# Kernel optimization log

Measured on AMD Instinct MI355X. Metric: run time of the kernel, lower is better.

The kernel has to match this reference:

```python
import jax, jax.numpy as jnp
import numpy as np

INPUT_DIM, LATENT_DIM, HIDDEN_DIM, BATCH = 1024, 128, 1024, 32768


def setup_inputs() -> dict:
    key = jax.random.key(0)
    ks = jax.random.split(key, 12)
    s = 0.02
    x = (jax.random.uniform(ks[0], (BATCH, INPUT_DIM)) < 0.5).astype(jnp.float32)  # binary data
    eps = jax.random.normal(ks[1], (BATCH, LATENT_DIM), dtype=jnp.float32)
    return {
        "x": x,
        "eps": eps,
        "We1": jax.random.normal(ks[2], (INPUT_DIM, HIDDEN_DIM)) * s,
        "be1": jnp.zeros((HIDDEN_DIM,), jnp.float32),
        "Wmu": jax.random.normal(ks[3], (HIDDEN_DIM, LATENT_DIM)) * s,
        "bmu": jnp.zeros((LATENT_DIM,), jnp.float32),
        "Wls": jax.random.normal(ks[4], (HIDDEN_DIM, LATENT_DIM)) * s,
        "bls": jnp.zeros((LATENT_DIM,), jnp.float32),
        "Wd1": jax.random.normal(ks[5], (LATENT_DIM, HIDDEN_DIM)) * s,
        "bd1": jnp.zeros((HIDDEN_DIM,), jnp.float32),
        "Wd2": jax.random.normal(ks[6], (HIDDEN_DIM, INPUT_DIM)) * s,
        "bd2": jnp.zeros((INPUT_DIM,), jnp.float32),
    }


def reference(x, eps, We1, be1, Wmu, bmu, Wls, bls, Wd1, bd1, Wd2, bd2):
    # Encoder: one hidden ReLU layer, mu / logsigma heads
    h = jax.nn.relu(x @ We1 + be1)                      # [B, H]
    mu = h @ Wmu + bmu                                  # [B, L]
    logsigma = h @ Wls + bls                            # [B, L]
    # Reparameterization: z = sigma * eps + mu (vectorized diag(exp(logsigma)) @ eps)
    z = mu + jnp.exp(logsigma) * eps                    # [B, L]
    # Decoder: one hidden ReLU layer, sigmoid Bernoulli params
    hd = jax.nn.relu(z @ Wd1 + bd1)                     # [B, H]
    theta = jax.nn.sigmoid(hd @ Wd2 + bd2)              # [B, D]
    # Bernoulli log-likelihood: sum_j log(theta^x * (1-theta)^(1-x))
    log_px = jnp.sum(x * jnp.log(theta) + (1.0 - x) * jnp.log1p(-theta), axis=-1)  # [B]
    # KL(q||N(0,I)) = 0.5 * sum(sigma^2 + mu^2 - log(sigma^2) - 1)
    kl = 0.5 * jnp.sum(jnp.exp(2.0 * logsigma) + mu * mu - 2.0 * logsigma - 1.0, axis=-1)  # [B]
    return log_px - kl                                  # elbo_mc [B]
```

## Files before the change

kernel.cpp:

```cpp
#include <hip/hip_runtime.h>
#include <cstdint>
#include <cstddef>


typedef __bf16 bf16x8 __attribute__((ext_vector_type(8)));
typedef float f32x4 __attribute__((ext_vector_type(4)));

__device__ __forceinline__ unsigned short f32_to_bf16(float f) {
  unsigned int u = __float_as_uint(f);
  u += 0x7fffu + ((u >> 16) & 1u);
  return (unsigned short)(u >> 16);
}

__global__ void cast_bf16_k(const float* __restrict__ in,
                            unsigned short* __restrict__ out,
                            unsigned short* __restrict__ xbit, int n4) {
  int stride = gridDim.x * blockDim.x;
  for (int i = blockIdx.x * blockDim.x + threadIdx.x; i < n4; i += stride) {
    float4 v = reinterpret_cast<const float4*>(in)[i];
    ushort4 o = make_ushort4(f32_to_bf16(v.x), f32_to_bf16(v.y),
                             f32_to_bf16(v.z), f32_to_bf16(v.w));
    reinterpret_cast<ushort4*>(out)[i] = o;
    unsigned int nib = (v.x != 0.f ? 1u : 0u) | (v.y != 0.f ? 2u : 0u) |
                       (v.z != 0.f ? 4u : 0u) | (v.w != 0.f ? 8u : 0u);
    unsigned int n1 = __shfl_down(nib, 1, 64);
    unsigned int n2 = __shfl_down(nib, 2, 64);
    unsigned int n3 = __shfl_down(nib, 3, 64);
    if ((threadIdx.x & 3) == 0)
      xbit[i >> 2] = (unsigned short)(nib | (n1 << 4) | (n2 << 8) | (n3 << 12));
  }
}

struct TransJob { const float* in; unsigned short* out; int K, N, blkEnd; };

__global__ void transpose_all_k(TransJob j0, TransJob j1, TransJob j2,
                                TransJob j3, TransJob j4) {
  __shared__ float tile[32][33];
  int bid = blockIdx.x;
  TransJob j; int base;
  if (bid < j0.blkEnd)      { j = j0; base = 0; }
  else if (bid < j1.blkEnd) { j = j1; base = j0.blkEnd; }
  else if (bid < j2.blkEnd) { j = j2; base = j1.blkEnd; }
  else if (bid < j3.blkEnd) { j = j3; base = j2.blkEnd; }
  else                      { j = j4; base = j3.blkEnd; }
  int local = bid - base;
  int gxN = j.N >> 5;
  int n0 = (local % gxN) * 32, k0 = (local / gxN) * 32;
  int tx = threadIdx.x, ty = threadIdx.y;
#pragma unroll
  for (int r = 0; r < 32; r += 8)
    tile[ty + r][tx] = j.in[(size_t)(k0 + ty + r) * j.N + n0 + tx];
  __syncthreads();
#pragma unroll
  for (int r = 0; r < 32; r += 8)
    j.out[(size_t)(n0 + ty + r) * j.K + k0 + tx] = f32_to_bf16(tile[tx][ty + r]);
}

__device__ __forceinline__ void gl_lds16(const unsigned short* g, unsigned short* l) {
  __builtin_amdgcn_global_load_lds(
      (__attribute__((address_space(1))) void*)g,
      (__attribute__((address_space(3))) void*)l, 16, 0, 0);
}

template <int EPI, int TAG>
__global__ __launch_bounds__(512, 2) void gemm256(
    const unsigned short* __restrict__ A, const unsigned short* __restrict__ BT,
    int gx, int N, int K,
    const float* __restrict__ bias0,
    unsigned short* __restrict__ outb, float* __restrict__ outf,
    const unsigned short* __restrict__ xbit) {
  __shared__ __align__(16) unsigned short lds[2][2][256 * 64];

  const int tid = threadIdx.x;
  const int lane = tid & 63;
  const int wave = tid >> 6;
  const int wr = wave >> 2;
  const int wc = wave & 3;
  const int lm = lane & 15, lq = lane >> 4;
  const int sw = lm & 7;

  const int bid = blockIdx.x;
  const int xcd = bid & 7;
  const int t8 = bid >> 3;
  const int m0 = (xcd + 8 * (t8 / gx)) * 256;
  const int n0 = (t8 % gx) * 256;
  const int NT = K >> 6;

  const unsigned short* gpA[2];
  const unsigned short* gpB[2];
  int loA[2], loB[2];
#pragma unroll
  for (int r = 0; r < 2; ++r) {
    int c = tid + 512 * r, rl = c >> 3, q8 = c & 7;
    int rowA = (rl & 63) + ((rl >> 6) << 7);
    int rowB = (rl & 31) + ((rl >> 5) << 6);
    gpA[r] = A + (size_t)(m0 + rowA) * K + (q8 ^ (rowA & 7)) * 8;
    gpB[r] = BT + (size_t)(n0 + rowB) * K + (q8 ^ (rowB & 7)) * 8;
    loA[r] = rowA * 64 + q8 * 8;
    loB[r] = rowB * 64 + q8 * 8;
  }

  auto stage = [&](int kind, int buf, int kt) {
#pragma unroll
    for (int r = 0; r < 2; ++r) {
      if (kind == 0)      gl_lds16(gpA[r] + kt * 64,          &lds[buf][0][loA[r]]);
      else if (kind == 3) gl_lds16(gpA[r] + 64 * K + kt * 64, &lds[buf][0][loA[r] + 64 * 64]);
      else if (kind == 1) gl_lds16(gpB[r] + kt * 64,          &lds[buf][1][loB[r]]);
      else                gl_lds16(gpB[r] + 32 * K + kt * 64, &lds[buf][1][loB[r] + 32 * 64]);
    }
  };

  stage(0, 0, 0); stage(1, 0, 0); stage(2, 0, 0); stage(3, 0, 0);
  stage(0, 1, 1); stage(1, 1, 1); stage(2, 1, 1);
  asm volatile("s_waitcnt vmcnt(6)" ::: "memory");
  __builtin_amdgcn_s_barrier();

  f32x4 acc[8][4] = {};

  const int aRow = (wr * 128 + lm) * 64;
  const int bRow = (wc * 64 + lm) * 64;
  const int c0 = ((0 | lq) ^ sw) * 8;
  const int c1 = ((4 | lq) ^ sw) * 8;

  for (int t = 0; t < NT; ++t) {
    const int b = t & 1;
    const unsigned short* Ab = &lds[b][0][0];
    const unsigned short* Bb = &lds[b][1][0];
    bf16x8 af[4][2], bf1[2][2], bf2[2][2];

#pragma unroll
    for (int i = 0; i < 4; ++i) {
      af[i][0] = *reinterpret_cast<const bf16x8*>(Ab + aRow + i * 1024 + c0);
      af[i][1] = *reinterpret_cast<const bf16x8*>(Ab + aRow + i * 1024 + c1);
    }
#pragma unroll
    for (int j = 0; j < 2; ++j) {
      bf1[j][0] = *reinterpret_cast<const bf16x8*>(Bb + bRow + j * 1024 + c0);
      bf1[j][1] = *reinterpret_cast<const bf16x8*>(Bb + bRow + j * 1024 + c1);
    }
    if (t + 1 < NT) stage(3, (t + 1) & 1, t + 1);
    __builtin_amdgcn_s_barrier();
    asm volatile("s_waitcnt lgkmcnt(0)" ::: "memory");
    __builtin_amdgcn_sched_barrier(0);
    __builtin_amdgcn_s_setprio(1);
#pragma unroll
    for (int s = 0; s < 2; ++s)
#pragma unroll
      for (int i = 0; i < 4; ++i)
#pragma unroll
        for (int j = 0; j < 2; ++j)
          acc[i][j] = __builtin_amdgcn_mfma_f32_16x16x32_bf16(af[i][s], bf1[j][s], acc[i][j], 0, 0, 0);
    __builtin_amdgcn_s_setprio(0);
    __builtin_amdgcn_s_barrier();

#pragma unroll
    for (int j = 0; j < 2; ++j) {
      bf2[j][0] = *reinterpret_cast<const bf16x8*>(Bb + bRow + (j + 2) * 1024 + c0);
      bf2[j][1] = *reinterpret_cast<const bf16x8*>(Bb + bRow + (j + 2) * 1024 + c1);
    }
    if (t + 2 < NT) stage(0, b, t + 2);
    __builtin_amdgcn_s_barrier();
    asm volatile("s_waitcnt lgkmcnt(0)" ::: "memory");
    __builtin_amdgcn_sched_barrier(0);
    __builtin_amdgcn_s_setprio(1);
#pragma unroll
    for (int s = 0; s < 2; ++s)
#pragma unroll
      for (int i = 0; i < 4; ++i)
#pragma unroll
        for (int j = 0; j < 2; ++j)
          acc[i][j + 2] = __builtin_amdgcn_mfma_f32_16x16x32_bf16(af[i][s], bf2[j][s], acc[i][j + 2], 0, 0, 0);
    __builtin_amdgcn_s_setprio(0);
    __builtin_amdgcn_s_barrier();

#pragma unroll
    for (int i = 0; i < 4; ++i) {
      af[i][0] = *reinterpret_cast<const bf16x8*>(Ab + aRow + (64 + i * 16) * 64 + c0);
      af[i][1] = *reinterpret_cast<const bf16x8*>(Ab + aRow + (64 + i * 16) * 64 + c1);
    }
    if (t + 2 < NT) stage(1, b, t + 2);
    __builtin_amdgcn_s_barrier();
    asm volatile("s_waitcnt lgkmcnt(0)" ::: "memory");
    __builtin_amdgcn_sched_barrier(0);
    __builtin_amdgcn_s_setprio(1);
#pragma unroll
    for (int s = 0; s < 2; ++s)
#pragma unroll
      for (int i = 0; i < 4; ++i)
#pragma unroll
        for (int j = 0; j < 2; ++j)
          acc[i + 4][j] = __builtin_amdgcn_mfma_f32_16x16x32_bf16(af[i][s], bf1[j][s], acc[i + 4][j], 0, 0, 0);
    __builtin_amdgcn_s_setprio(0);
    __builtin_amdgcn_s_barrier();

    if (t + 2 < NT) stage(2, b, t + 2);
    __builtin_amdgcn_s_barrier();
    __builtin_amdgcn_s_setprio(1);
#pragma unroll
    for (int s = 0; s < 2; ++s)
#pragma unroll
      for (int i = 0; i < 4; ++i)
#pragma unroll
        for (int j = 0; j < 2; ++j)
          acc[i + 4][j + 2] = __builtin_amdgcn_mfma_f32_16x16x32_bf16(af[i][s], bf2[j][s], acc[i + 4][j + 2], 0, 0, 0);
    __builtin_amdgcn_s_setprio(0);
    if (t + 2 < NT)      { asm volatile("s_waitcnt vmcnt(6)" ::: "memory"); }
    else if (t + 1 < NT) { asm volatile("s_waitcnt vmcnt(0)" ::: "memory"); }
    __builtin_amdgcn_s_barrier();
  }

  if (EPI == 0) {
#pragma unroll
    for (int i = 0; i < 8; ++i)
#pragma unroll
      for (int j = 0; j < 4; ++j) {
        int col = n0 + wc * 64 + j * 16 + lm;
        float bias = bias0[col];
#pragma unroll
        for (int r = 0; r < 4; ++r) {
          int row = m0 + wr * 128 + i * 16 + lq * 4 + r;
          float v = acc[i][j][r] + bias;
          outb[(size_t)row * N + col] = f32_to_bf16(fmaxf(v, 0.f));
        }
      }
  } else {
    const int wpr = N >> 4;
#pragma unroll
    for (int i = 0; i < 8; ++i) {
      float rs[4] = {0.f, 0.f, 0.f, 0.f};
#pragma unroll
      for (int j = 0; j < 4; ++j) {
        int col = n0 + wc * 64 + j * 16 + lm;
        float bias = bias0[col];
        int w16 = (col >> 4);
#pragma unroll
        for (int r = 0; r < 4; ++r) {
          int row = m0 + wr * 128 + i * 16 + lq * 4 + r;
          float l = acc[i][j][r] + bias;
          unsigned short mask = xbit[(size_t)row * wpr + w16];
          float tt = ((mask >> lm) & 1) ? -l : l;
          float sp = fmaxf(tt, 0.f) + __logf(1.f + __expf(-fabsf(tt)));
          rs[r] -= sp;
        }
      }
#pragma unroll
      for (int off = 1; off < 16; off <<= 1)
#pragma unroll
        for (int r = 0; r < 4; ++r) rs[r] += __shfl_xor(rs[r], off, 64);
      if (lm == 0) {
#pragma unroll
        for (int r = 0; r < 4; ++r)
          atomicAdd(&outf[m0 + wr * 128 + i * 16 + lq * 4 + r], rs[r]);
      }
    }
  }
}

__global__ __launch_bounds__(256, 1) void latent_fused(
    const unsigned short* A,
    const unsigned short* __restrict__ BT,
    const unsigned short* __restrict__ WD1,
    const float* __restrict__ bmu, const float* __restrict__ bls,
    const float* __restrict__ bd1,
    const float* __restrict__ eps,
    unsigned short* hd,
    float* __restrict__ out) {
  __shared__ __align__(16) unsigned short smem[49152];
  unsigned short* As  = smem;
  unsigned short* Bs  = smem + 8192;
  unsigned short* Bs2 = smem;
  unsigned short* zs  = smem + 32768;

  const int K = 1024;
  const int tid = threadIdx.x;
  const int lane = tid & 63;
  const int wave = tid >> 6;
  const int m0 = blockIdx.x * 128;
  const int lm = lane & 15, lq = lane >> 4;
  const int sw = lm & 7;

  const unsigned short* agp[4];
  const unsigned short* bgp[8];
#pragma unroll
  for (int r = 0; r < 4; ++r) {
    int c = tid + 256 * r;
    int row = c >> 3, q = (c & 7) ^ (row & 7);
    agp[r] = A + (size_t)(m0 + row) * K + q * 8;
  }
#pragma unroll
  for (int r = 0; r < 8; ++r) {
    int c = tid + 256 * r;
    int row = c >> 3, q = (c & 7) ^ (row & 7);
    bgp[r] = BT + (size_t)row * K + q * 8;
  }

  f32x4 acc[2][16] = {};

  for (int kt = 0; kt < K; kt += 64) {
#pragma unroll
    for (int r = 0; r < 4; ++r) gl_lds16(agp[r] + kt, As + (tid + 256 * r) * 8);
#pragma unroll
    for (int r = 0; r < 8; ++r) gl_lds16(bgp[r] + kt, Bs + (tid + 256 * r) * 8);
    __syncthreads();

#pragma unroll
    for (int s = 0; s < 2; ++s) {
      const int so = ((s << 2) | lq) ^ sw;
      bf16x8 af[2];
#pragma unroll
      for (int i = 0; i < 2; ++i)
        af[i] = *reinterpret_cast<const bf16x8*>(As + (wave * 32 + i * 16 + lm) * 64 + so * 8);
#pragma unroll
      for (int j = 0; j < 16; ++j) {
        bf16x8 b = *reinterpret_cast<const bf16x8*>(Bs + (j * 16 + lm) * 64 + so * 8);
        acc[0][j] = __builtin_amdgcn_mfma_f32_16x16x32_bf16(af[0], b, acc[0][j], 0, 0, 0);
        acc[1][j] = __builtin_amdgcn_mfma_f32_16x16x32_bf16(af[1], b, acc[1][j], 0, 0, 0);
      }
    }
    __syncthreads();
  }

  auto stage2 = [&](int nt) {
#pragma unroll
    for (int ri = 0; ri < 16; ++ri) {
      int c = tid + 256 * ri;
      int row = c >> 4, slot = c & 15;
      int gc = slot ^ (row & 7);
      gl_lds16(WD1 + (size_t)(nt * 256 + row) * 128 + gc * 8, Bs2 + c * 8);
    }
  };
  stage2(0);

#pragma unroll
  for (int i = 0; i < 2; ++i) {
    float kl[4] = {0.f, 0.f, 0.f, 0.f};
#pragma unroll
    for (int j = 0; j < 8; ++j) {
      int dim = j * 16 + lm;
      float bm = bmu[dim], bl = bls[dim];
#pragma unroll
      for (int r = 0; r < 4; ++r) {
        int rowl = wave * 32 + i * 16 + lq * 4 + r;
        float mu = acc[i][j][r] + bm;
        float ls = acc[i][j + 8][r] + bl;
        float e = eps[(size_t)(m0 + rowl) * 128 + dim];
        float zv = fmaf(__expf(ls), e, mu);
        int chunk = (dim >> 3);
        int slot = chunk ^ (rowl & 7);
        zs[rowl * 128 + slot * 8 + (lm & 7)] = f32_to_bf16(zv);
        kl[r] += 0.5f * (__expf(2.f * ls) + mu * mu - 2.f * ls - 1.f);
      }
    }
#pragma unroll
    for (int off = 1; off < 16; off <<= 1)
#pragma unroll
      for (int r = 0; r < 4; ++r) kl[r] += __shfl_xor(kl[r], off, 64);
    if (lm == 0) {
#pragma unroll
      for (int r = 0; r < 4; ++r)
        out[m0 + wave * 32 + i * 16 + lq * 4 + r] = -kl[r];
    }
  }

  for (int nt = 0; nt < 4; ++nt) {
    asm volatile("s_waitcnt vmcnt(0)" ::: "memory");
    __syncthreads();
    f32x4 acc2[2][16] = {};
#pragma unroll
    for (int ks = 0; ks < 4; ++ks) {
      const int cks = (ks * 4 + lq) ^ (lm & 7);
      bf16x8 a0 = *reinterpret_cast<const bf16x8*>(zs + (wave * 32 + lm) * 128 + cks * 8);
      bf16x8 a1 = *reinterpret_cast<const bf16x8*>(zs + (wave * 32 + 16 + lm) * 128 + cks * 8);
#pragma unroll
      for (int j = 0; j < 16; ++j) {
        bf16x8 b = *reinterpret_cast<const bf16x8*>(Bs2 + (j * 16 + lm) * 128 + cks * 8);
        acc2[0][j] = __builtin_amdgcn_mfma_f32_16x16x32_bf16(a0, b, acc2[0][j], 0, 0, 0);
        acc2[1][j] = __builtin_amdgcn_mfma_f32_16x16x32_bf16(a1, b, acc2[1][j], 0, 0, 0);
      }
    }
    __syncthreads();
    if (nt + 1 < 4) stage2(nt + 1);
#pragma unroll
    for (int i = 0; i < 2; ++i)
#pragma unroll
      for (int j = 0; j < 16; ++j) {
        int col = nt * 256 + j * 16 + lm;
        float bias = bd1[col];
#pragma unroll
        for (int r = 0; r < 4; ++r) {
          int row = m0 + wave * 32 + i * 16 + lq * 4 + r;
          float v = acc2[i][j][r] + bias;
          hd[(size_t)row * 1024 + col] = f32_to_bf16(fmaxf(v, 0.f));
        }
      }
  }
}

extern "C" void kernel_launch(void* const* d_in, const int* in_sizes, int n_in,
                              void* d_out, int out_size, void* d_ws, size_t ws_size,
                              hipStream_t stream) {
  const float* x   = (const float*)d_in[0];
  const float* eps = (const float*)d_in[1];
  const float* We1 = (const float*)d_in[2];
  const float* be1 = (const float*)d_in[3];
  const float* Wmu = (const float*)d_in[4];
  const float* bmu = (const float*)d_in[5];
  const float* Wls = (const float*)d_in[6];
  const float* bls = (const float*)d_in[7];
  const float* Wd1 = (const float*)d_in[8];
  const float* bd1 = (const float*)d_in[9];
  const float* Wd2 = (const float*)d_in[10];
  const float* bd2 = (const float*)d_in[11];
  float* out = (float*)d_out;

  const int B = 32768, D = 1024, H = 1024, L = 128;

  char* ws = (char*)d_ws;
  size_t off = 0;
  auto alloc = [&](size_t bytes) {
    void* p = ws + off;
    off += (bytes + 255) & ~(size_t)255;
    return p;
  };
  unsigned short* xbf  = (unsigned short*)alloc((size_t)B * D * 2);
  unsigned short* xbit = (unsigned short*)alloc((size_t)B * D / 8);
  unsigned short* w1t  = (unsigned short*)alloc((size_t)H * D * 2);
  unsigned short* w2t  = (unsigned short*)alloc((size_t)256 * H * 2);
  unsigned short* wd1t = (unsigned short*)alloc((size_t)H * L * 2);
  unsigned short* wd2t = (unsigned short*)alloc((size_t)D * H * 2);
  unsigned short* h    = (unsigned short*)alloc((size_t)B * H * 2);
  unsigned short* hd   = h;

  cast_bf16_k<<<2048, 256, 0, stream>>>(x, xbf, xbit, B * D / 4);

  TransJob j0{We1, w1t, D, H, 1024};
  TransJob j1{Wmu, w2t, H, L, 1152};
  TransJob j2{Wls, w2t + 128 * H, H, L, 1280};
  TransJob j3{Wd1, wd1t, L, H, 1408};
  TransJob j4{Wd2, wd2t, H, D, 2432};
  transpose_all_k<<<2432, dim3(32, 8), 0, stream>>>(j0, j1, j2, j3, j4);

  gemm256<0, 1><<<512, 512, 0, stream>>>(
      xbf, w1t, 4, H, D, be1, h, nullptr, nullptr);
  latent_fused<<<B / 128, 256, 0, stream>>>(
      h, w2t, wd1t, bmu, bls, bd1, eps, hd, out);
  gemm256<2, 4><<<512, 512, 0, stream>>>(
      hd, wd2t, 4, D, H, bd2, nullptr, out, xbit);

  (void)in_sizes; (void)n_in; (void)out_size; (void)ws_size;
}
```

Baseline: 444.8 us.

## Merge cast and transpose prep kernels; double-buffer latent GEMM loads

Folds the x-to-bf16 cast and bit-packing into the weight transpose launch, giving one prep kernel instead of two and removing a launch and its serialization gap. In latent_fused, the K-loop now uses double-buffered LDS tiles: the next tile's global-to-LDS loads are issued before computing on the current tile, to overlap memory with MFMA work. LDS use grows from 96KB to 128KB per block, which may limit occupancy. The loop-end syncthreads is presumably retained to protect buffer reuse.

New measurement: 440.8 us. No clear change (-0.9%).

```diff
diff --git a/kernel.cpp b/kernel.cpp
--- a/kernel.cpp
+++ b/kernel.cpp
@@ -12,31 +12,35 @@
   return (unsigned short)(u >> 16);
 }
 
-__global__ void cast_bf16_k(const float* __restrict__ in,
-                            unsigned short* __restrict__ out,
-                            unsigned short* __restrict__ xbit, int n4) {
-  int stride = gridDim.x * blockDim.x;
-  for (int i = blockIdx.x * blockDim.x + threadIdx.x; i < n4; i += stride) {
-    float4 v = reinterpret_cast<const float4*>(in)[i];
-    ushort4 o = make_ushort4(f32_to_bf16(v.x), f32_to_bf16(v.y),
-                             f32_to_bf16(v.z), f32_to_bf16(v.w));
-    reinterpret_cast<ushort4*>(out)[i] = o;
-    unsigned int nib = (v.x != 0.f ? 1u : 0u) | (v.y != 0.f ? 2u : 0u) |
-                       (v.z != 0.f ? 4u : 0u) | (v.w != 0.f ? 8u : 0u);
-    unsigned int n1 = __shfl_down(nib, 1, 64);
-    unsigned int n2 = __shfl_down(nib, 2, 64);
-    unsigned int n3 = __shfl_down(nib, 3, 64);
-    if ((threadIdx.x & 3) == 0)
-      xbit[i >> 2] = (unsigned short)(nib | (n1 << 4) | (n2 << 8) | (n3 << 12));
-  }
-}
-
 struct TransJob { const float* in; unsigned short* out; int K, N, blkEnd; };
 
-__global__ void transpose_all_k(TransJob j0, TransJob j1, TransJob j2,
-                                TransJob j3, TransJob j4) {
+__global__ void prep_k(TransJob j0, TransJob j1, TransJob j2,
+                       TransJob j3, TransJob j4,
+                       const float* __restrict__ x,
+                       unsigned short* __restrict__ xbf,
+                       unsigned short* __restrict__ xbit,
+                       int n4, int castBlocks) {
   __shared__ float tile[32][33];
   int bid = blockIdx.x;
+  int tx = threadIdx.x, ty = threadIdx.y;
+  if (bid >= j4.blkEnd) {
+    int tid = ty * 32 + tx;
+    int stride = castBlocks * 256;
+    for (int i = (bid - j4.blkEnd) * 256 + tid; i < n4; i += stride) {
+      float4 v = reinterpret_cast<const float4*>(x)[i];
+      ushort4 o = make_ushort4(f32_to_bf16(v.x), f32_to_bf16(v.y),
+                               f32_to_bf16(v.z), f32_to_bf16(v.w));
+      reinterpret_cast<ushort4*>(xbf)[i] = o;
+      unsigned int nib = (v.x != 0.f ? 1u : 0u) | (v.y != 0.f ? 2u : 0u) |
+                         (v.z != 0.f ? 4u : 0u) | (v.w != 0.f ? 8u : 0u);
+      unsigned int n1 = __shfl_down(nib, 1, 64);
+      unsigned int n2 = __shfl_down(nib, 2, 64);
+      unsigned int n3 = __shfl_down(nib, 3, 64);
+      if ((tid & 3) == 0)
+        xbit[i >> 2] = (unsigned short)(nib | (n1 << 4) | (n2 << 8) | (n3 << 12));
+    }
+    return;
+  }
   TransJob j; int base;
   if (bid < j0.blkEnd)      { j = j0; base = 0; }
   else if (bid < j1.blkEnd) { j = j1; base = j0.blkEnd; }
@@ -46,7 +50,6 @@
   int local = bid - base;
   int gxN = j.N >> 5;
   int n0 = (local % gxN) * 32, k0 = (local / gxN) * 32;
-  int tx = threadIdx.x, ty = threadIdx.y;
 #pragma unroll
   for (int r = 0; r < 32; r += 8)
     tile[ty + r][tx] = j.in[(size_t)(k0 + ty + r) * j.N + n0 + tx];
@@ -265,11 +268,13 @@
     const float* __restrict__ eps,
     unsigned short* hd,
     float* __restrict__ out) {
-  __shared__ __align__(16) unsigned short smem[49152];
-  unsigned short* As  = smem;
-  unsigned short* Bs  = smem + 8192;
+  __shared__ __align__(16) unsigned short smem[65536];
+  unsigned short* As0 = smem;
+  unsigned short* As1 = smem + 8192;
+  unsigned short* Bs0 = smem + 16384;
+  unsigned short* Bs1 = smem + 32768;
+  unsigned short* zs  = smem + 49152;
   unsigned short* Bs2 = smem;
-  unsigned short* zs  = smem + 32768;
 
   const int K = 1024;
   const int tid = threadIdx.x;
@@ -294,25 +299,35 @@
     bgp[r] = BT + (size_t)row * K + q * 8;
   }
 
+  auto stage1 = [&](int buf, int kt) {
+    unsigned short* Ad = buf ? As1 : As0;
+    unsigned short* Bd = buf ? Bs1 : Bs0;
+#pragma unroll
+    for (int r = 0; r < 4; ++r) gl_lds16(agp[r] + kt, Ad + (tid + 256 * r) * 8);
+#pragma unroll
+    for (int r = 0; r < 8; ++r) gl_lds16(bgp[r] + kt, Bd + (tid + 256 * r) * 8);
+  };
+
   f32x4 acc[2][16] = {};
 
-  for (int kt = 0; kt < K; kt += 64) {
-#pragma unroll
-    for (int r = 0; r < 4; ++r) gl_lds16(agp[r] + kt, As + (tid + 256 * r) * 8);
-#pragma unroll
-    for (int r = 0; r < 8; ++r) gl_lds16(bgp[r] + kt, Bs + (tid + 256 * r) * 8);
-    __syncthreads();
-
+  stage1(0, 0);
+  __syncthreads();
+
+  for (int t = 0; t < 16; ++t) {
+    const int cur = t & 1;
+    if (t + 1 < 16) stage1(cur ^ 1, (t + 1) * 64);
+    const unsigned short* Ab = cur ? As1 : As0;
+    const unsigned short* Bb = cur ? Bs1 : Bs0;
 #pragma unroll
     for (int s = 0; s < 2; ++s) {
       const int so = ((s << 2) | lq) ^ sw;
       bf16x8 af[2];
 #pragma unroll
       for (int i = 0; i < 2; ++i)
-        af[i] = *reinterpret_cast<const bf16x8*>(As + (wave * 32 + i * 16 + lm) * 64 + so * 8);
+        af[i] = *reinterpret_cast<const bf16x8*>(Ab + (wave * 32 + i * 16 + lm) * 64 + so * 8);
 #pragma unroll
       for (int j = 0; j < 16; ++j) {
-        bf16x8 b = *reinterpret_cast<const bf16x8*>(Bs + (j * 16 + lm) * 64 + so * 8);
+        bf16x8 b = *reinterpret_cast<const bf16x8*>(Bb + (j * 16 + lm) * 64 + so * 8);
         acc[0][j] = __builtin_amdgcn_mfma_f32_16x16x32_bf16(af[0], b, acc[0][j], 0, 0, 0);
         acc[1][j] = __builtin_amdgcn_mfma_f32_16x16x32_bf16(af[1], b, acc[1][j], 0, 0, 0);
       }
@@ -431,14 +446,13 @@
   unsigned short* h    = (unsigned short*)alloc((size_t)B * H * 2);
   unsigned short* hd   = h;
 
-  cast_bf16_k<<<2048, 256, 0, stream>>>(x, xbf, xbit, B * D / 4);
-
   TransJob j0{We1, w1t, D, H, 1024};
   TransJob j1{Wmu, w2t, H, L, 1152};
   TransJob j2{Wls, w2t + 128 * H, H, L, 1280};
   TransJob j3{Wd1, wd1t, L, H, 1408};
   TransJob j4{Wd2, wd2t, H, D, 2432};
-  transpose_all_k<<<2432, dim3(32, 8), 0, stream>>>(j0, j1, j2, j3, j4);
+  prep_k<<<2432 + 2048, dim3(32, 8), 0, stream>>>(
+      j0, j1, j2, j3, j4, x, xbf, xbit, B * D / 4, 2048);
 
   gemm256<0, 1><<<512, 512, 0, stream>>>(
       xbf, w1t, 4, H, D, be1, h, nullptr, nullptr);
```
